# Kernel optimization log

Hardware: AMD Instinct MI355X
Metric: run time of the kernel (lower is better)

## Reference

```python
import jax, jax.numpy as jnp
import numpy as np

B, S, D = 16, 2048, 128

def setup_inputs() -> dict:
    key = jax.random.key(0)
    kq, kk, kv, km = jax.random.split(key, 4)
    Q = jax.random.normal(kq, (B, S, D), dtype=jnp.float32)
    K = jax.random.normal(kk, (B, S, D), dtype=jnp.float32)
    V = jax.random.normal(kv, (B, S, D), dtype=jnp.float32)
    # mask: True entries are masked out (filled with -inf), same as torch.masked_fill_
    mask = jax.random.randint(km, (B, S, S), 0, 2).astype(bool)
    return {"Q": Q, "K": K, "V": V, "mask": mask, "dk": 128}

def reference(Q, K, V, mask, dk):
    # scores: [B, S_q, S_k]
    w = jnp.einsum('bqd,bkd->bqk', Q, K)
    w = jnp.where(mask, -jnp.inf, w)
    # scale applied to masked scores (as in original: mask first, then divide);
    # -inf / scale stays -inf, so math matches exactly.
    scale = jnp.asarray(dk, w.dtype) ** 0.5
    p = jax.nn.softmax(w / scale, axis=-1)
    # context: [B, S_q, D]
    return jnp.einsum('bqk,bkd->bqd', p, V)
```

## Files before the change

kernel.cpp:

```cpp
#include <hip/hip_runtime.h>
#include <hip/hip_bf16.h>
#include <stdint.h>

typedef __attribute__((ext_vector_type(8))) short short8;
typedef __attribute__((ext_vector_type(4))) float floatx4;

#define S_LEN 2048
#define DH    128
#define BQ    64
#define BKV   64
#define NSTEP (S_LEN / BKV)
#define SCALE 0.08838834764831845f
#define SCALE2 0.12753785429791905f
#define DTHR 11.541560327111708f

__device__ __forceinline__ float ex2(float x) { return __builtin_amdgcn_exp2f(x); }

__device__ __forceinline__ unsigned short f2b(float f) {
    union { float f; unsigned u; } v; v.f = f;
    unsigned r = v.u + 0x7fffu + ((v.u >> 16) & 1u);
    return (unsigned short)(r >> 16);
}

__device__ __forceinline__ unsigned cvt_pk(float lo, float hi) {
    unsigned r;
    asm("v_cvt_pk_bf16_f32 %0, %1, %2" : "=v"(r) : "v"(lo), "v"(hi));
    return r;
}

__device__ __forceinline__ void gll16(const void* g, void* l) {
    __builtin_amdgcn_global_load_lds(
        (__attribute__((address_space(1))) void*)(g),
        (__attribute__((address_space(3))) void*)(l), 16, 0, 0);
}


__global__ __launch_bounds__(256) void conv_k(const float* __restrict__ K,
                                              unsigned short* __restrict__ Kbf)
{
    int i = blockIdx.x * 256 + threadIdx.x;
    float4 v = ((const float4*)K)[i];
    ushort4 o;
    o.x = f2b(v.x); o.y = f2b(v.y); o.z = f2b(v.z); o.w = f2b(v.w);
    ((ushort4*)Kbf)[i] = o;
}

__global__ __launch_bounds__(256) void transp_v(const float* __restrict__ V,
                                                unsigned short* __restrict__ Vt)
{
    __shared__ float t[32][33];
    const int k0 = blockIdx.x * 32, d0 = blockIdx.y * 32, b = blockIdx.z;
    const int tx = threadIdx.x & 31, ty = threadIdx.x >> 5;
    const float* Vb = V + ((size_t)b * S_LEN + k0) * DH + d0;
    #pragma unroll
    for (int i = 0; i < 4; ++i)
        t[ty + 8 * i][tx] = Vb[(size_t)(ty + 8 * i) * DH + tx];
    __syncthreads();
    unsigned short* Vtb = Vt + ((size_t)b * DH + d0) * S_LEN + k0;
    #pragma unroll
    for (int i = 0; i < 4; ++i)
        Vtb[(size_t)(ty + 8 * i) * S_LEN + tx] = f2b(t[tx][ty + 8 * i]);
}

#define LDS_BYTES 77824

__global__ __launch_bounds__(256, 2)
void attn_fwd(const float* __restrict__ Q, const unsigned short* __restrict__ Kbf,
              const unsigned short* __restrict__ Vt, const int* __restrict__ M,
              float* __restrict__ O)
{
    __shared__ __align__(128) char lds[LDS_BYTES];

    const int tid  = threadIdx.x;
    const int lane = tid & 63;
    const int w    = tid >> 6;
    const int c    = lane & 15;
    const int g    = lane >> 4;
    const int qt   = blockIdx.x;
    const int b    = blockIdx.y;
    const int q0   = qt * BQ;

    const int vd = tid & 127;
    const int vh = tid >> 7;
    const int krow_l = lane >> 4;
    const int kcol_l = (lane & 15) * 16;

    short8 qf[4];
    {
        const float* qrow = Q + ((size_t)(b * S_LEN + q0 + w * 16 + c)) * DH;
        #pragma unroll
        for (int dk = 0; dk < 4; ++dk) {
            const float* p = qrow + dk * 32 + g * 8;
            float4 a  = *(const float4*)(p);
            float4 bb = *(const float4*)(p + 4);
            short8 f;
            f[0] = f2b(a.x * SCALE2);  f[1] = f2b(a.y * SCALE2);
            f[2] = f2b(a.z * SCALE2);  f[3] = f2b(a.w * SCALE2);
            f[4] = f2b(bb.x * SCALE2); f[5] = f2b(bb.y * SCALE2);
            f[6] = f2b(bb.z * SCALE2); f[7] = f2b(bb.w * SCALE2);
            qf[dk] = f;
        }
    }

    float m_run = -1e30f;
    float l_run = 0.f;
    floatx4 accO[8];
    #pragma unroll
    for (int i = 0; i < 8; ++i) accO[i] = (floatx4)(0.f);

    const char*           Kb8 = (const char*)(Kbf + (size_t)b * S_LEN * DH);
    const unsigned short* Vtb = Vt + (size_t)b * DH * S_LEN;
    const int* Mrow = M + (size_t)b * S_LEN * S_LEN
                        + (size_t)(q0 + w * 16 + c) * S_LEN + 4 * g;

    short8 vreg[4];
    int4   mregA[4], mregB[4];
    char*  psw = lds + 69632 + w * 2048;

#define LOAD_MASK(DST, TT) {                                                  \
    const int* mp_ = Mrow + (TT) * BKV;                                       \
    DST[0] = *(const int4*)(mp_);                                             \
    DST[1] = *(const int4*)(mp_ + 16);                                        \
    DST[2] = *(const int4*)(mp_ + 32);                                        \
    DST[3] = *(const int4*)(mp_ + 48); }

    #pragma unroll
    for (int i = 0; i < 4; ++i) {
        int j = (w << 2) | i;
        int r = 4 * j + krow_l;
        unsigned cb = (unsigned)kcol_l ^ (unsigned)((r & 7) << 4);
        gll16(Kb8 + (size_t)r * 256 + cb, lds + j * 1024);
    }
    #pragma unroll
    for (int j = 0; j < 4; ++j)
        vreg[j] = *(const short8*)(Vtb + (size_t)vd * S_LEN + vh * 32 + j * 8);
    #pragma unroll
    for (int j = 0; j < 4; ++j)
        *(short8*)(lds + 32768 + vd * 144 + vh * 64 + j * 16) = vreg[j];
    #pragma unroll
    for (int j = 0; j < 4; ++j)
        vreg[j] = *(const short8*)(Vtb + (size_t)vd * S_LEN + BKV + vh * 32 + j * 8);
    LOAD_MASK(mregA, 0);
    LOAD_MASK(mregB, 1);
    __syncthreads();

#define STEP_BODY(T, MCUR) {                                                  \
    const int pb  = (T) & 1;                                                  \
    const int kv0 = (T) * BKV;                                                \
                 \
    if ((T) + 1 < NSTEP) {                                                    \
        const char* Ksrc = Kb8 + (size_t)(kv0 + BKV) * 256;                   \
        char* KHn = lds + ((pb ^ 1) * 16384);                                 \
        _Pragma("unroll")                                                     \
        for (int i = 0; i < 4; ++i) {                                         \
            int j = (w << 2) | i;                                             \
            int r = 4 * j + krow_l;                                           \
            unsigned cb = (unsigned)kcol_l ^ (unsigned)((r & 7) << 4);        \
            gll16(Ksrc + (size_t)r * 256 + cb, KHn + j * 1024);               \
        }                                                                     \
    }                                                                         \
                                       \
    if ((T) + 1 < NSTEP) {                                                    \
        _Pragma("unroll")                                                     \
        for (int j = 0; j < 4; ++j)                                           \
            *(short8*)(lds + 32768 + (pb ^ 1) * 18432 + vd * 144 + vh * 64    \
                       + j * 16) = vreg[j];                                   \
    }                                                                         \
                                                     \
    if ((T) + 2 < NSTEP) {                                                    \
        const unsigned short* vs_ = Vtb + (size_t)vd * S_LEN                  \
                                   + (kv0 + 2 * BKV) + vh * 32;               \
        _Pragma("unroll")                                                     \
        for (int j = 0; j < 4; ++j)                                           \
            vreg[j] = *(const short8*)(vs_ + j * 8);                          \
    }                                                                         \
                               \
    floatx4 accS[4];                                                          \
    _Pragma("unroll")                                                         \
    for (int n = 0; n < 4; ++n) accS[n] = (floatx4)(0.f);                     \
    {                                                                         \
        const char* KHp = lds + pb * 16384;                                   \
        __builtin_amdgcn_s_setprio(1);                                        \
        _Pragma("unroll")                                                     \
        for (int n = 0; n < 4; ++n) {                                         \
            const char* krow = KHp + (n * 16 + c) * 256;                      \
            _Pragma("unroll")                                                 \
            for (int dk = 0; dk < 4; ++dk) {                                  \
                short8 kf = *(const short8*)(krow +                           \
                    ((unsigned)(dk * 64 + g * 16) ^ (unsigned)((c & 7) << 4)));\
                accS[n] = __builtin_amdgcn_mfma_f32_16x16x32_bf16(            \
                              kf, qf[dk], accS[n], 0, 0, 0);                  \
            }                                                                 \
        }                                                                     \
        __builtin_amdgcn_s_setprio(0);                                        \
    }                                                                         \
                                \
    float p_[4][4];                                                           \
    _Pragma("unroll")                                                         \
    for (int n = 0; n < 4; ++n) {                                             \
        int4 mm = MCUR[n];                                                    \
        p_[n][0] = mm.x ? -1e30f : accS[n][0];                                \
        p_[n][1] = mm.y ? -1e30f : accS[n][1];                                \
        p_[n][2] = mm.z ? -1e30f : accS[n][2];                                \
        p_[n][3] = mm.w ? -1e30f : accS[n][3];                                \
    }                                                                         \
    float mx = p_[0][0];                                                      \
    _Pragma("unroll")                                                         \
    for (int n = 0; n < 4; ++n)                                               \
        _Pragma("unroll")                                                     \
        for (int r = 0; r < 4; ++r) mx = fmaxf(mx, p_[n][r]);                 \
    mx = fmaxf(mx, __shfl_xor(mx, 16));                                       \
    mx = fmaxf(mx, __shfl_xor(mx, 32));                                       \
    int need = __any(mx - m_run > DTHR);                                      \
    float corr = 1.0f;                                                        \
    if (need) {                                                               \
        float mn = fmaxf(m_run, mx);                                          \
        corr = ex2(m_run - mn);                                               \
        m_run = mn;                                                           \
    }                                                                         \
    float ts = 0.f;                                                           \
    _Pragma("unroll")                                                         \
    for (int n = 0; n < 4; ++n)                                               \
        _Pragma("unroll")                                                     \
        for (int r = 0; r < 4; ++r) {                                         \
            p_[n][r] = ex2(p_[n][r] - m_run);                                 \
            ts += p_[n][r];                                                   \
        }                                                                     \
    ts += __shfl_xor(ts, 16);                                                 \
    ts += __shfl_xor(ts, 32);                                                 \
    if (need) {                                                               \
        l_run = l_run * corr + ts;                                            \
        _Pragma("unroll")                                                     \
        for (int s8 = 0; s8 < 8; ++s8) {                                      \
            floatx4 o = accO[s8];                                             \
            o[0] *= corr; o[1] *= corr; o[2] *= corr; o[3] *= corr;           \
            accO[s8] = o;                                                     \
        }                                                                     \
    } else {                                                                  \
        l_run += ts;                                                          \
    }                                                                         \
                                                       \
    if ((T) + 2 < NSTEP) LOAD_MASK(MCUR, (T) + 2);                            \
                \
    _Pragma("unroll")                                                         \
    for (int n = 0; n < 4; ++n) {                                             \
        unsigned w0 = cvt_pk(p_[n][0], p_[n][1]);                             \
        unsigned w1 = cvt_pk(p_[n][2], p_[n][3]);                             \
        unsigned long long pk = (unsigned long long)w0                        \
                              | ((unsigned long long)w1 << 32);               \
        *(unsigned long long*)(psw + (4 * n + g) * 128                        \
                               + ((c * 8) ^ (g << 3))) = pk;                  \
    }                                                                         \
                     \
    {                                                                         \
        const char* VTp = lds + 32768 + pb * 18432;                           \
        _Pragma("unroll")                                                     \
        for (int sub = 0; sub < 2; ++sub) {                                   \
            int ra = 8 * sub + 2 * g;                                         \
            unsigned long long lo = *(const unsigned long long*)(psw + ra*128 \
                                    + ((c * 8) ^ ((ra & 3) << 3)));           \
            unsigned long long hi = *(const unsigned long long*)(psw          \
                                    + (ra + 1) * 128                          \
                                    + ((c * 8) ^ (((ra + 1) & 3) << 3)));     \
            union { unsigned long long q[2]; short8 v; } pu;                  \
            pu.q[0] = lo; pu.q[1] = hi;                                       \
            short8 pf = pu.v;                                                 \
            __builtin_amdgcn_s_setprio(1);                                    \
            _Pragma("unroll")                                                 \
            for (int s8 = 0; s8 < 8; ++s8) {                                  \
                short8 vf = *(const short8*)(VTp + (s8 * 16 + c) * 144        \
                                             + sub * 64 + g * 16);            \
                accO[s8] = __builtin_amdgcn_mfma_f32_16x16x32_bf16(           \
                               vf, pf, accO[s8], 0, 0, 0);                    \
            }                                                                 \
            __builtin_amdgcn_s_setprio(0);                                    \
        }                                                                     \
    }                                                                         \
    __syncthreads(); }

    for (int t = 0; t < NSTEP; t += 2) {
        STEP_BODY(t,     mregA)
        STEP_BODY(t + 1, mregB)
    }
#undef STEP_BODY
#undef LOAD_MASK

    float inv = (l_run > 0.f) ? 1.f / l_run : 0.f;
    float* Ob = O + ((size_t)(b * S_LEN + q0 + w * 16 + c)) * DH;
    #pragma unroll
    for (int s8 = 0; s8 < 8; ++s8) {
        float4 ov;
        ov.x = accO[s8][0] * inv; ov.y = accO[s8][1] * inv;
        ov.z = accO[s8][2] * inv; ov.w = accO[s8][3] * inv;
        *(float4*)(Ob + s8 * 16 + 4 * g) = ov;
    }
}

#define FB_LDS_BYTES 77824

__global__ __launch_bounds__(256, 2)
void attn_fwd_fb(const float* __restrict__ Q, const float* __restrict__ K,
                 const float* __restrict__ V, const int* __restrict__ M,
                 float* __restrict__ O)
{
    __shared__ __align__(128) char lds[FB_LDS_BYTES];

    const int tid  = threadIdx.x;
    const int lane = tid & 63;
    const int w    = tid >> 6;
    const int c    = lane & 15;
    const int g    = lane >> 4;
    const int qt   = blockIdx.x;
    const int b    = blockIdx.y;
    const int q0   = qt * BQ;

    const int rbase = tid >> 5;
    const int c4    = tid & 31;
    const unsigned swk = (unsigned)(c4 * 8) ^ (unsigned)(rbase << 4);
    const int vd    = tid & 127;
    const int vk0   = (tid >> 7) * 32;

    short8 qf[4];
    {
        const float* qrow = Q + ((size_t)(b * S_LEN + q0 + w * 16 + c)) * DH;
        #pragma unroll
        for (int dk = 0; dk < 4; ++dk) {
            const float* p = qrow + dk * 32 + g * 8;
            float4 a  = *(const float4*)(p);
            float4 bb = *(const float4*)(p + 4);
            short8 f;
            f[0] = f2b(a.x * SCALE);  f[1] = f2b(a.y * SCALE);
            f[2] = f2b(a.z * SCALE);  f[3] = f2b(a.w * SCALE);
            f[4] = f2b(bb.x * SCALE); f[5] = f2b(bb.y * SCALE);
            f[6] = f2b(bb.z * SCALE); f[7] = f2b(bb.w * SCALE);
            qf[dk] = f;
        }
    }

    float m_run[4] = {-1e30f, -1e30f, -1e30f, -1e30f};
    float l_run[4] = {0.f, 0.f, 0.f, 0.f};
    floatx4 accO[8];
    #pragma unroll
    for (int i = 0; i < 8; ++i) accO[i] = (floatx4)(0.f);

    const float* Kb = K + (size_t)b * S_LEN * DH;
    const float* Vb = V + (size_t)b * S_LEN * DH;
    const int*   Mb = M + (size_t)b * S_LEN * S_LEN + (size_t)q0 * S_LEN;

    size_t moff[4];
    #pragma unroll
    for (int r = 0; r < 4; ++r)
        moff[r] = (size_t)(w * 16 + 4 * g + r) * S_LEN;

    float4 kreg[8];
    float  vreg[32];
    int    mreg[16];

    #pragma unroll
    for (int i = 0; i < 8; ++i)
        kreg[i] = *(const float4*)(Kb + (size_t)(i * 8 + rbase) * DH + c4 * 4);
    #pragma unroll
    for (int j = 0; j < 32; ++j)
        vreg[j] = Vb[(size_t)(vk0 + j) * DH + vd];
    #pragma unroll
    for (int r = 0; r < 4; ++r)
        #pragma unroll
        for (int n = 0; n < 4; ++n)
            mreg[r * 4 + n] = Mb[moff[r] + n * 16 + c];

    #pragma unroll
    for (int i = 0; i < 8; ++i) {
        float4 kv = kreg[i];
        unsigned long long kp =
              (unsigned long long)f2b(kv.x)
            | ((unsigned long long)f2b(kv.y) << 16)
            | ((unsigned long long)f2b(kv.z) << 32)
            | ((unsigned long long)f2b(kv.w) << 48);
        *(unsigned long long*)(lds + (i * 8 + rbase) * 256 + swk) = kp;
    }
    {
        char* vbase = lds + 32768 + vd * 144 + vk0 * 2;
        #pragma unroll
        for (int i = 0; i < 4; ++i) {
            short8 pk;
            #pragma unroll
            for (int e = 0; e < 8; ++e) pk[e] = f2b(vreg[i * 8 + e]);
            *(short8*)(vbase + i * 16) = pk;
        }
    }
    #pragma unroll
    for (int i = 0; i < 8; ++i)
        kreg[i] = *(const float4*)(Kb + (size_t)(BKV + i * 8 + rbase) * DH + c4 * 4);
    #pragma unroll
    for (int j = 0; j < 32; ++j)
        vreg[j] = Vb[(size_t)(BKV + vk0 + j) * DH + vd];

    __syncthreads();

    char* psw = lds + 69632 + w * 2048;

    for (int step = 0; step < NSTEP; ++step) {
        const int p = step & 1;
        const int kv0 = step * BKV;
        char* KHp = lds + p * 16384;
        char* VTp = lds + 32768 + p * 18432;

        floatx4 accS[4];
        #pragma unroll
        for (int n = 0; n < 4; ++n) accS[n] = (floatx4)(0.f);
        #pragma unroll
        for (int n = 0; n < 4; ++n) {
            const char* krow = KHp + (n * 16 + c) * 256;
            #pragma unroll
            for (int dk = 0; dk < 4; ++dk) {
                unsigned colb = (unsigned)(dk * 64 + g * 16) ^ (unsigned)((c & 7) << 4);
                short8 kf = *(const short8*)(krow + colb);
                accS[n] = __builtin_amdgcn_mfma_f32_16x16x32_bf16(qf[dk], kf, accS[n], 0, 0, 0);
            }
        }

        float pv[4][4];
        float corr[4];
        #pragma unroll
        for (int r = 0; r < 4; ++r) {
            float sv[4];
            #pragma unroll
            for (int n = 0; n < 4; ++n) {
                float s = accS[n][r];
                if (mreg[r * 4 + n]) s = -1e30f;
                sv[n] = s;
            }
            float tm = fmaxf(fmaxf(sv[0], sv[1]), fmaxf(sv[2], sv[3]));
            #pragma unroll
            for (int off = 1; off < 16; off <<= 1)
                tm = fmaxf(tm, __shfl_xor(tm, off, 64));
            float mn = fmaxf(m_run[r], tm);
            corr[r]  = __expf(m_run[r] - mn);
            m_run[r] = mn;
            float ts = 0.f;
            #pragma unroll
            for (int n = 0; n < 4; ++n) { pv[n][r] = __expf(sv[n] - mn); ts += pv[n][r]; }
            #pragma unroll
            for (int off = 1; off < 16; off <<= 1)
                ts += __shfl_xor(ts, off, 64);
            l_run[r] = l_run[r] * corr[r] + ts;
        }
        if (step + 1 < NSTEP) {
            const int kvn = kv0 + BKV;
            #pragma unroll
            for (int r = 0; r < 4; ++r)
                #pragma unroll
                for (int n = 0; n < 4; ++n)
                    mreg[r * 4 + n] = Mb[moff[r] + kvn + n * 16 + c];
        }

        #pragma unroll
        for (int s8 = 0; s8 < 8; ++s8) {
            floatx4 o = accO[s8];
            o[0] *= corr[0]; o[1] *= corr[1]; o[2] *= corr[2]; o[3] *= corr[3];
            accO[s8] = o;
        }

        #pragma unroll
        for (int r = 0; r < 4; ++r) {
            int rl = 4 * g + r;
            #pragma unroll
            for (int n = 0; n < 4; ++n) {
                unsigned colb = (unsigned)((n * 16 + c) * 2) ^ (unsigned)((rl & 7) << 4);
                *(unsigned short*)(psw + rl * 128 + colb) = f2b(pv[n][r]);
            }
        }

        #pragma unroll
        for (int sub = 0; sub < 2; ++sub) {
            unsigned colb = (unsigned)(sub * 64 + g * 16) ^ (unsigned)((c & 7) << 4);
            short8 pf = *(const short8*)(psw + c * 128 + colb);
            #pragma unroll
            for (int s8 = 0; s8 < 8; ++s8) {
                short8 vf = *(const short8*)(VTp + (s8 * 16 + c) * 144 + sub * 64 + g * 16);
                accO[s8] = __builtin_amdgcn_mfma_f32_16x16x32_bf16(pf, vf, accO[s8], 0, 0, 0);
            }
        }

        if (step + 1 < NSTEP) {
            char* KHn = lds + (p ^ 1) * 16384;
            char* VTn = lds + 32768 + (p ^ 1) * 18432;
            #pragma unroll
            for (int i = 0; i < 8; ++i) {
                float4 kv = kreg[i];
                unsigned long long kp =
                      (unsigned long long)f2b(kv.x)
                    | ((unsigned long long)f2b(kv.y) << 16)
                    | ((unsigned long long)f2b(kv.z) << 32)
                    | ((unsigned long long)f2b(kv.w) << 48);
                *(unsigned long long*)(KHn + (i * 8 + rbase) * 256 + swk) = kp;
            }
            char* vbase = VTn + vd * 144 + vk0 * 2;
            #pragma unroll
            for (int i = 0; i < 4; ++i) {
                short8 pk;
                #pragma unroll
                for (int e = 0; e < 8; ++e) pk[e] = f2b(vreg[i * 8 + e]);
                *(short8*)(vbase + i * 16) = pk;
            }
            if (step + 2 < NSTEP) {
                const int kvn2 = kv0 + 2 * BKV;
                #pragma unroll
                for (int i = 0; i < 8; ++i)
                    kreg[i] = *(const float4*)(Kb + (size_t)(kvn2 + i * 8 + rbase) * DH + c4 * 4);
                #pragma unroll
                for (int j = 0; j < 32; ++j)
                    vreg[j] = Vb[(size_t)(kvn2 + vk0 + j) * DH + vd];
            }
        }
        __syncthreads();
    }

    float inv[4];
    #pragma unroll
    for (int r = 0; r < 4; ++r) inv[r] = (l_run[r] > 0.f) ? 1.f / l_run[r] : 0.f;
    float* Ob = O + ((size_t)(b * S_LEN + q0 + w * 16)) * DH;
    #pragma unroll
    for (int s8 = 0; s8 < 8; ++s8) {
        #pragma unroll
        for (int r = 0; r < 4; ++r) {
            Ob[(size_t)(4 * g + r) * DH + s8 * 16 + c] = accO[s8][r] * inv[r];
        }
    }
}

extern "C" void kernel_launch(void* const* d_in, const int* in_sizes, int n_in,
                              void* d_out, int out_size, void* d_ws, size_t ws_size,
                              hipStream_t stream) {
    const float* Q = (const float*)d_in[0];
    const float* K = (const float*)d_in[1];
    const float* V = (const float*)d_in[2];
    const int*   M = (const int*)d_in[3];
    float*       O = (float*)d_out;

    const size_t elems = (size_t)16 * S_LEN * DH;
    if (ws_size >= 2 * elems * sizeof(unsigned short)) {
        unsigned short* Kbf = (unsigned short*)d_ws;
        unsigned short* Vt  = (unsigned short*)d_ws + elems;
        conv_k<<<dim3((unsigned)(elems / 4 / 256)), dim3(256), 0, stream>>>(K, Kbf);
        transp_v<<<dim3(S_LEN / 32, DH / 32, 16), dim3(256), 0, stream>>>(V, Vt);
        attn_fwd<<<dim3(S_LEN / BQ, 16), dim3(256), 0, stream>>>(Q, Kbf, Vt, M, O);
    } else {
        attn_fwd_fb<<<dim3(S_LEN / BQ, 16), dim3(256), 0, stream>>>(Q, K, V, M, O);
    }
}
```

Baseline: 115.5 us.

## Double query rows per wave to reuse K/V tiles across two Q subtiles

Each wave now handles 32 query rows (two 16-row subtiles) instead of 16, so the block covers 128 queries and every K fragment and V fragment loaded from LDS feeds two MFMAs. This halves K/V global and LDS traffic per query. Mask prefetch changes from two-step-ahead double registers to one-step-ahead for both subtiles. In exchange, register pressure roughly doubles for accumulators, occupancy drops to one block per CU, and the grid halves to 256 blocks, which may underfill the GPU.

```diff
diff --git a/kernel.cpp b/kernel.cpp
--- a/kernel.cpp
+++ b/kernel.cpp
@@ -7,7 +7,7 @@
 
 #define S_LEN 2048
 #define DH    128
-#define BQ    64
+#define BQ    128
 #define BKV   64
 #define NSTEP (S_LEN / BKV)
 #define SCALE 0.08838834764831845f
@@ -62,9 +62,9 @@
         Vtb[(size_t)(ty + 8 * i) * S_LEN + tx] = f2b(t[tx][ty + 8 * i]);
 }
 
-#define LDS_BYTES 77824
-
-__global__ __launch_bounds__(256, 2)
+#define LDS_BYTES 86016
+
+__global__ __launch_bounds__(256, 1)
 void attn_fwd(const float* __restrict__ Q, const unsigned short* __restrict__ Kbf,
               const unsigned short* __restrict__ Vt, const int* __restrict__ M,
               float* __restrict__ O)
@@ -85,9 +85,10 @@
     const int krow_l = lane >> 4;
     const int kcol_l = (lane & 15) * 16;
 
-    short8 qf[4];
-    {
-        const float* qrow = Q + ((size_t)(b * S_LEN + q0 + w * 16 + c)) * DH;
+    short8 qf[2][4];
+    #pragma unroll
+    for (int qs = 0; qs < 2; ++qs) {
+        const float* qrow = Q + ((size_t)(b * S_LEN + q0 + w * 32 + qs * 16 + c)) * DH;
         #pragma unroll
         for (int dk = 0; dk < 4; ++dk) {
             const float* p = qrow + dk * 32 + g * 8;
@@ -98,31 +99,33 @@
             f[2] = f2b(a.z * SCALE2);  f[3] = f2b(a.w * SCALE2);
             f[4] = f2b(bb.x * SCALE2); f[5] = f2b(bb.y * SCALE2);
             f[6] = f2b(bb.z * SCALE2); f[7] = f2b(bb.w * SCALE2);
-            qf[dk] = f;
-        }
-    }
-
-    float m_run = -1e30f;
-    float l_run = 0.f;
-    floatx4 accO[8];
-    #pragma unroll
-    for (int i = 0; i < 8; ++i) accO[i] = (floatx4)(0.f);
+            qf[qs][dk] = f;
+        }
+    }
+
+    float m_run[2] = {-1e30f, -1e30f};
+    float l_run[2] = {0.f, 0.f};
+    floatx4 accO0[8], accO1[8];
+    #pragma unroll
+    for (int i = 0; i < 8; ++i) { accO0[i] = (floatx4)(0.f); accO1[i] = (floatx4)(0.f); }
 
     const char*           Kb8 = (const char*)(Kbf + (size_t)b * S_LEN * DH);
     const unsigned short* Vtb = Vt + (size_t)b * DH * S_LEN;
-    const int* Mrow = M + (size_t)b * S_LEN * S_LEN
-                        + (size_t)(q0 + w * 16 + c) * S_LEN + 4 * g;
+    const int* Mrow0 = M + (size_t)b * S_LEN * S_LEN
+                         + (size_t)(q0 + w * 32 + c) * S_LEN + 4 * g;
+    const int* Mrow1 = Mrow0 + (size_t)16 * S_LEN;
 
     short8 vreg[4];
-    int4   mregA[4], mregB[4];
-    char*  psw = lds + 69632 + w * 2048;
-
-#define LOAD_MASK(DST, TT) {                                                  \
-    const int* mp_ = Mrow + (TT) * BKV;                                       \
-    DST[0] = *(const int4*)(mp_);                                             \
-    DST[1] = *(const int4*)(mp_ + 16);                                        \
-    DST[2] = *(const int4*)(mp_ + 32);                                        \
-    DST[3] = *(const int4*)(mp_ + 48); }
+    int4   mcur[8];
+    char*  psw = lds + 69632 + w * 4096;
+
+#define LOAD_MASK(TT) {                                                       \
+    const int* m0_ = Mrow0 + (TT) * BKV;                                      \
+    const int* m1_ = Mrow1 + (TT) * BKV;                                      \
+    mcur[0] = *(const int4*)(m0_);      mcur[1] = *(const int4*)(m0_ + 16);   \
+    mcur[2] = *(const int4*)(m0_ + 32); mcur[3] = *(const int4*)(m0_ + 48);   \
+    mcur[4] = *(const int4*)(m1_);      mcur[5] = *(const int4*)(m1_ + 16);   \
+    mcur[6] = *(const int4*)(m1_ + 32); mcur[7] = *(const int4*)(m1_ + 48); }
 
     #pragma unroll
     for (int i = 0; i < 4; ++i) {
@@ -140,14 +143,13 @@
     #pragma unroll
     for (int j = 0; j < 4; ++j)
         vreg[j] = *(const short8*)(Vtb + (size_t)vd * S_LEN + BKV + vh * 32 + j * 8);
-    LOAD_MASK(mregA, 0);
-    LOAD_MASK(mregB, 1);
+    LOAD_MASK(0);
     __syncthreads();
 
-#define STEP_BODY(T, MCUR) {                                                  \
+#define STEP_BODY(T) {                                                        \
     const int pb  = (T) & 1;                                                  \
     const int kv0 = (T) * BKV;                                                \
-                 \
+                                                  \
     if ((T) + 1 < NSTEP) {                                                    \
         const char* Ksrc = Kb8 + (size_t)(kv0 + BKV) * 256;                   \
         char* KHn = lds + ((pb ^ 1) * 16384);                                 \
@@ -159,14 +161,13 @@
             gll16(Ksrc + (size_t)r * 256 + cb, KHn + j * 1024);               \
         }                                                                     \
     }                                                                         \
-                                       \
+                            \
     if ((T) + 1 < NSTEP) {                                                    \
         _Pragma("unroll")                                                     \
         for (int j = 0; j < 4; ++j)                                           \
             *(short8*)(lds + 32768 + (pb ^ 1) * 18432 + vd * 144 + vh * 64    \
                        + j * 16) = vreg[j];                                   \
     }                                                                         \
-                                                     \
     if ((T) + 2 < NSTEP) {                                                    \
         const unsigned short* vs_ = Vtb + (size_t)vd * S_LEN                  \
                                    + (kv0 + 2 * BKV) + vh * 32;               \
@@ -174,10 +175,11 @@
         for (int j = 0; j < 4; ++j)                                           \
             vreg[j] = *(const short8*)(vs_ + j * 8);                          \
     }                                                                         \
-                               \
-    floatx4 accS[4];                                                          \
+                                      \
+    floatx4 accS[2][4];                                                       \
     _Pragma("unroll")                                                         \
-    for (int n = 0; n < 4; ++n) accS[n] = (floatx4)(0.f);                     \
+    for (int n = 0; n < 4; ++n) { accS[0][n] = (floatx4)(0.f);                \
+                                  accS[1][n] = (floatx4)(0.f); }              \
     {                                                                         \
         const char* KHp = lds + pb * 16384;                                   \
         __builtin_amdgcn_s_setprio(1);                                        \
@@ -188,111 +190,134 @@
             for (int dk = 0; dk < 4; ++dk) {                                  \
                 short8 kf = *(const short8*)(krow +                           \
                     ((unsigned)(dk * 64 + g * 16) ^ (unsigned)((c & 7) << 4)));\
-                accS[n] = __builtin_amdgcn_mfma_f32_16x16x32_bf16(            \
-                              kf, qf[dk], accS[n], 0, 0, 0);                  \
+                accS[0][n] = __builtin_amdgcn_mfma_f32_16x16x32_bf16(         \
+                                 kf, qf[0][dk], accS[0][n], 0, 0, 0);         \
+                accS[1][n] = __builtin_amdgcn_mfma_f32_16x16x32_bf16(         \
+                                 kf, qf[1][dk], accS[1][n], 0, 0, 0);         \
             }                                                                 \
         }                                                                     \
         __builtin_amdgcn_s_setprio(0);                                        \
     }                                                                         \
-                                \
-    float p_[4][4];                                                           \
+                  \
     _Pragma("unroll")                                                         \
-    for (int n = 0; n < 4; ++n) {                                             \
-        int4 mm = MCUR[n];                                                    \
-        p_[n][0] = mm.x ? -1e30f : accS[n][0];                                \
-        p_[n][1] = mm.y ? -1e30f : accS[n][1];                                \
-        p_[n][2] = mm.z ? -1e30f : accS[n][2];                                \
-        p_[n][3] = mm.w ? -1e30f : accS[n][3];                                \
-    }                                                                         \
-    float mx = p_[0][0];                                                      \
-    _Pragma("unroll")                                                         \
-    for (int n = 0; n < 4; ++n)                                               \
-        _Pragma("unroll")                                                     \
-        for (int r = 0; r < 4; ++r) mx = fmaxf(mx, p_[n][r]);                 \
-    mx = fmaxf(mx, __shfl_xor(mx, 16));                                       \
-    mx = fmaxf(mx, __shfl_xor(mx, 32));                                       \
-    int need = __any(mx - m_run > DTHR);                                      \
-    float corr = 1.0f;                                                        \
-    if (need) {                                                               \
-        float mn = fmaxf(m_run, mx);                                          \
-        corr = ex2(m_run - mn);                                               \
-        m_run = mn;                                                           \
-    }                                                                         \
-    float ts = 0.f;                                                           \
-    _Pragma("unroll")                                                         \
-    for (int n = 0; n < 4; ++n)                                               \
-        _Pragma("unroll")                                                     \
-        for (int r = 0; r < 4; ++r) {                                         \
-            p_[n][r] = ex2(p_[n][r] - m_run);                                 \
-            ts += p_[n][r];                                                   \
-        }                                                                     \
-    ts += __shfl_xor(ts, 16);                                                 \
-    ts += __shfl_xor(ts, 32);                                                 \
-    if (need) {                                                               \
-        l_run = l_run * corr + ts;                                            \
-        _Pragma("unroll")                                                     \
-        for (int s8 = 0; s8 < 8; ++s8) {                                      \
-            floatx4 o = accO[s8];                                             \
-            o[0] *= corr; o[1] *= corr; o[2] *= corr; o[3] *= corr;           \
-            accO[s8] = o;                                                     \
-        }                                                                     \
-    } else {                                                                  \
-        l_run += ts;                                                          \
-    }                                                                         \
-                                                       \
-    if ((T) + 2 < NSTEP) LOAD_MASK(MCUR, (T) + 2);                            \
-                \
-    _Pragma("unroll")                                                         \
-    for (int n = 0; n < 4; ++n) {                                             \
-        unsigned w0 = cvt_pk(p_[n][0], p_[n][1]);                             \
-        unsigned w1 = cvt_pk(p_[n][2], p_[n][3]);                             \
-        unsigned long long pk = (unsigned long long)w0                        \
-                              | ((unsigned long long)w1 << 32);               \
-        *(unsigned long long*)(psw + (4 * n + g) * 128                        \
-                               + ((c * 8) ^ (g << 3))) = pk;                  \
+    for (int qs = 0; qs < 2; ++qs) {                                          \
+        float p_[4][4];                                                       \
+        _Pragma("unroll")                                                     \
+        for (int n = 0; n < 4; ++n) {                                         \
+            int4 mm = mcur[qs * 4 + n];                                       \
+            p_[n][0] = mm.x ? -1e30f : accS[qs][n][0];                        \
+            p_[n][1] = mm.y ? -1e30f : accS[qs][n][1];                        \
+            p_[n][2] = mm.z ? -1e30f : accS[qs][n][2];                        \
+            p_[n][3] = mm.w ? -1e30f : accS[qs][n][3];                        \
+        }                                                                     \
+        float mx = p_[0][0];                                                  \
+        _Pragma("unroll")                                                     \
+        for (int n = 0; n < 4; ++n)                                           \
+            _Pragma("unroll")                                                 \
+            for (int r = 0; r < 4; ++r) mx = fmaxf(mx, p_[n][r]);             \
+        mx = fmaxf(mx, __shfl_xor(mx, 16));                                   \
+        mx = fmaxf(mx, __shfl_xor(mx, 32));                                   \
+        int need = __any(mx - m_run[qs] > DTHR);                              \
+        float corr = 1.0f;                                                    \
+        if (need) {                                                           \
+            float mn = fmaxf(m_run[qs], mx);                                  \
+            corr = ex2(m_run[qs] - mn);                                       \
+            m_run[qs] = mn;                                                   \
+        }                                                                     \
+        float ts = 0.f;                                                       \
+        _Pragma("unroll")                                                     \
+        for (int n = 0; n < 4; ++n)                                           \
+            _Pragma("unroll")                                                 \
+            for (int r = 0; r < 4; ++r) {                                     \
+                p_[n][r] = ex2(p_[n][r] - m_run[qs]);                         \
+                ts += p_[n][r];                                               \
+            }                                                                 \
+        ts += __shfl_xor(ts, 16);                                             \
+        ts += __shfl_xor(ts, 32);                                             \
+        if (need) {                                                           \
+            l_run[qs] = l_run[qs] * corr + ts;                                \
+            if (qs == 0) {                                                    \
+                _Pragma("unroll")                                             \
+                for (int s8 = 0; s8 < 8; ++s8) {                              \
+                    floatx4 o = accO0[s8];                                    \
+                    o[0] *= corr; o[1] *= corr; o[2] *= corr; o[3] *= corr;   \
+                    accO0[s8] = o;                                            \
+                }                                                             \
+            } else {                                                          \
+                _Pragma("unroll")                                             \
+                for (int s8 = 0; s8 < 8; ++s8) {                              \
+                    floatx4 o = accO1[s8];                                    \
+                    o[0] *= corr; o[1] *= corr; o[2] *= corr; o[3] *= corr;   \
+                    accO1[s8] = o;                                            \
+                }                                                             \
+            }                                                                 \
+        } else {                                                              \
+            l_run[qs] += ts;                                                  \
+        }                                                                     \
+                  \
+        _Pragma("unroll")                                                     \
+        for (int n = 0; n < 4; ++n) {                                         \
+            unsigned w0 = cvt_pk(p_[n][0], p_[n][1]);                         \
+            unsigned w1 = cvt_pk(p_[n][2], p_[n][3]);                         \
+            unsigned long long pk = (unsigned long long)w0                    \
+                                  | ((unsigned long long)w1 << 32);           \
+            *(unsigned long long*)(psw + qs * 2048 + (4 * n + g) * 128        \
+                                   + ((c * 8) ^ (g << 3))) = pk;              \
+        }                                                                     \
     }                                                                         \
                      \
+    if ((T) + 1 < NSTEP) LOAD_MASK((T) + 1);                                  \
+                                        \
     {                                                                         \
         const char* VTp = lds + 32768 + pb * 18432;                           \
         _Pragma("unroll")                                                     \
         for (int sub = 0; sub < 2; ++sub) {                                   \
             int ra = 8 * sub + 2 * g;                                         \
-            unsigned long long lo = *(const unsigned long long*)(psw + ra*128 \
-                                    + ((c * 8) ^ ((ra & 3) << 3)));           \
-            unsigned long long hi = *(const unsigned long long*)(psw          \
-                                    + (ra + 1) * 128                          \
-                                    + ((c * 8) ^ (((ra + 1) & 3) << 3)));     \
-            union { unsigned long long q[2]; short8 v; } pu;                  \
-            pu.q[0] = lo; pu.q[1] = hi;                                       \
-            short8 pf = pu.v;                                                 \
+            short8 pf[2];                                                     \
+            _Pragma("unroll")                                                 \
+            for (int qs = 0; qs < 2; ++qs) {                                  \
+                unsigned long long lo = *(const unsigned long long*)(psw      \
+                    + qs * 2048 + ra * 128 + ((c * 8) ^ ((ra & 3) << 3)));    \
+                unsigned long long hi = *(const unsigned long long*)(psw      \
+                    + qs * 2048 + (ra + 1) * 128                              \
+                    + ((c * 8) ^ (((ra + 1) & 3) << 3)));                     \
+                union { unsigned long long q[2]; short8 v; } pu;              \
+                pu.q[0] = lo; pu.q[1] = hi;                                   \
+                pf[qs] = pu.v;                                                \
+            }                                                                 \
             __builtin_amdgcn_s_setprio(1);                                    \
             _Pragma("unroll")                                                 \
             for (int s8 = 0; s8 < 8; ++s8) {                                  \
                 short8 vf = *(const short8*)(VTp + (s8 * 16 + c) * 144        \
                                              + sub * 64 + g * 16);            \
-                accO[s8] = __builtin_amdgcn_mfma_f32_16x16x32_bf16(           \
-                               vf, pf, accO[s8], 0, 0, 0);                    \
+                accO0[s8] = __builtin_amdgcn_mfma_f32_16x16x32_bf16(          \
+                               vf, pf[0], accO0[s8], 0, 0, 0);                \
+                accO1[s8] = __builtin_amdgcn_mfma_f32_16x16x32_bf16(          \
+                               vf, pf[1], accO1[s8], 0, 0, 0);                \
             }                                                                 \
             __builtin_amdgcn_s_setprio(0);                                    \
         }                                                                     \
     }                                                                         \
     __syncthreads(); }
 
-    for (int t = 0; t < NSTEP; t += 2) {
-        STEP_BODY(t,     mregA)
-        STEP_BODY(t + 1, mregB)
+    for (int t = 0; t < NSTEP; ++t) {
+        STEP_BODY(t)
     }
 #undef STEP_BODY
 #undef LOAD_MASK
 
-    float inv = (l_run > 0.f) ? 1.f / l_run : 0.f;
-    float* Ob = O + ((size_t)(b * S_LEN + q0 + w * 16 + c)) * DH;
-    #pragma unroll
-    for (int s8 = 0; s8 < 8; ++s8) {
-        float4 ov;
-        ov.x = accO[s8][0] * inv; ov.y = accO[s8][1] * inv;
-        ov.z = accO[s8][2] * inv; ov.w = accO[s8][3] * inv;
-        *(float4*)(Ob + s8 * 16 + 4 * g) = ov;
+    #pragma unroll
+    for (int qs = 0; qs < 2; ++qs) {
+        float inv = (l_run[qs] > 0.f) ? 1.f / l_run[qs] : 0.f;
+        float* Ob = O + ((size_t)(b * S_LEN + q0 + w * 32 + qs * 16 + c)) * DH;
+        #pragma unroll
+        for (int s8 = 0; s8 < 8; ++s8) {
+            floatx4 a = qs ? accO1[s8] : accO0[s8];
+            float4 ov;
+            ov.x = a[0] * inv; ov.y = a[1] * inv;
+            ov.z = a[2] * inv; ov.w = a[3] * inv;
+            *(float4*)(Ob + s8 * 16 + 4 * g) = ov;
+        }
     }
 }
 
@@ -312,7 +337,7 @@
     const int g    = lane >> 4;
     const int qt   = blockIdx.x;
     const int b    = blockIdx.y;
-    const int q0   = qt * BQ;
+    const int q0   = qt * 64;
 
     const int rbase = tid >> 5;
     const int c4    = tid & 31;
@@ -546,6 +571,6 @@
         transp_v<<<dim3(S_LEN / 32, DH / 32, 16), dim3(256), 0, stream>>>(V, Vt);
         attn_fwd<<<dim3(S_LEN / BQ, 16), dim3(256), 0, stream>>>(Q, Kbf, Vt, M, O);
     } else {
-        attn_fwd_fb<<<dim3(S_LEN / BQ, 16), dim3(256), 0, stream>>>(Q, K, V, M, O);
-    }
-}
+        attn_fwd_fb<<<dim3(S_LEN / 64, 16), dim3(256), 0, stream>>>(Q, K, V, M, O);
+    }
+}
```

Result: slower. 126.9 us (+9.9%).

## Switch attention to 32x32 MFMA with KV-split waves and register P transpose

Applied to the files above, without the earlier changes.

Rewrites the main attention kernel to use 32x32x16 bf16 MFMA. The four waves are split into two query halves times two KV halves, and the two KV-half partial results are merged through LDS at the end. The P tile is repacked with cross-lane shuffles instead of a per-wave LDS round trip, which lets the P staging buffer be dropped and reduces LDS use. The intent is fewer MFMA and LDS instructions per step, at the cost of a final merge, larger accumulator register pressure, and mask loads now issued only one step ahead.

```diff
diff --git a/kernel.cpp b/kernel.cpp
--- a/kernel.cpp
+++ b/kernel.cpp
@@ -2,8 +2,9 @@
 #include <hip/hip_bf16.h>
 #include <stdint.h>
 
-typedef __attribute__((ext_vector_type(8))) short short8;
-typedef __attribute__((ext_vector_type(4))) float floatx4;
+typedef __attribute__((ext_vector_type(8)))  short short8;
+typedef __attribute__((ext_vector_type(4)))  float floatx4;
+typedef __attribute__((ext_vector_type(16))) float floatx16;
 
 #define S_LEN 2048
 #define DH    128
@@ -62,7 +63,7 @@
         Vtb[(size_t)(ty + 8 * i) * S_LEN + tx] = f2b(t[tx][ty + 8 * i]);
 }
 
-#define LDS_BYTES 77824
+#define LDS_BYTES 69632
 
 __global__ __launch_bounds__(256, 2)
 void attn_fwd(const float* __restrict__ Q, const unsigned short* __restrict__ Kbf,
@@ -70,6 +71,255 @@
               float* __restrict__ O)
 {
     __shared__ __align__(128) char lds[LDS_BYTES];
+
+    const int tid  = threadIdx.x;
+    const int lane = tid & 63;
+    const int w    = tid >> 6;
+    const int wq   = w & 1;
+    const int wk   = w >> 1;
+    const int lq   = lane & 31;
+    const int hi   = lane >> 5;
+    const int qt   = blockIdx.x;
+    const int b    = blockIdx.y;
+    const int q0   = qt * BQ;
+
+    const int vd = tid & 127;
+    const int vh = tid >> 7;
+    const int krow_l = lane >> 4;
+    const int kcol_l = (lane & 15) * 16;
+
+    short8 qf[8];
+    {
+        const float* qrow = Q + ((size_t)(b * S_LEN + q0 + wq * 32 + lq)) * DH;
+        #pragma unroll
+        for (int dsub = 0; dsub < 8; ++dsub) {
+            const float* p = qrow + dsub * 16 + hi * 8;
+            float4 a  = *(const float4*)(p);
+            float4 bb = *(const float4*)(p + 4);
+            short8 f;
+            f[0] = f2b(a.x * SCALE2);  f[1] = f2b(a.y * SCALE2);
+            f[2] = f2b(a.z * SCALE2);  f[3] = f2b(a.w * SCALE2);
+            f[4] = f2b(bb.x * SCALE2); f[5] = f2b(bb.y * SCALE2);
+            f[6] = f2b(bb.z * SCALE2); f[7] = f2b(bb.w * SCALE2);
+            qf[dsub] = f;
+        }
+    }
+
+    float m_run = -1e30f;
+    float l_run = 0.f;
+    floatx16 accO[4];
+    #pragma unroll
+    for (int i = 0; i < 4; ++i) accO[i] = (floatx16)(0.f);
+
+    const char*           Kb8 = (const char*)(Kbf + (size_t)b * S_LEN * DH);
+    const unsigned short* Vtb = Vt + (size_t)b * DH * S_LEN;
+    const int* Mrow = M + (size_t)b * S_LEN * S_LEN
+                        + (size_t)(q0 + wq * 32 + lq) * S_LEN + wk * 32 + 4 * hi;
+
+    short8 vreg[4];
+    int4   mcur[4];
+
+#define LOAD_MASK(TT) {                                                       \
+    const int* mp_ = Mrow + (TT) * BKV;                                       \
+    mcur[0] = *(const int4*)(mp_);                                            \
+    mcur[1] = *(const int4*)(mp_ + 8);                                        \
+    mcur[2] = *(const int4*)(mp_ + 16);                                       \
+    mcur[3] = *(const int4*)(mp_ + 24); }
+
+    #pragma unroll
+    for (int i = 0; i < 4; ++i) {
+        int j = (w << 2) | i;
+        int r = 4 * j + krow_l;
+        unsigned cb = (unsigned)kcol_l ^ (unsigned)((r & 15) << 4);
+        gll16(Kb8 + (size_t)r * 256 + cb, lds + j * 1024);
+    }
+    #pragma unroll
+    for (int j = 0; j < 4; ++j)
+        vreg[j] = *(const short8*)(Vtb + (size_t)vd * S_LEN + vh * 32 + j * 8);
+    #pragma unroll
+    for (int j = 0; j < 4; ++j)
+        *(short8*)(lds + 32768 + vd * 144 + vh * 64 + j * 16) = vreg[j];
+    #pragma unroll
+    for (int j = 0; j < 4; ++j)
+        vreg[j] = *(const short8*)(Vtb + (size_t)vd * S_LEN + BKV + vh * 32 + j * 8);
+    LOAD_MASK(0);
+    __syncthreads();
+
+#define STEP_BODY(T) {                                                        \
+    const int pb  = (T) & 1;                                                  \
+    const int kv0 = (T) * BKV;                                                \
+                                                  \
+    if ((T) + 1 < NSTEP) {                                                    \
+        const char* Ksrc = Kb8 + (size_t)(kv0 + BKV) * 256;                   \
+        char* KHn = lds + ((pb ^ 1) * 16384);                                 \
+        _Pragma("unroll")                                                     \
+        for (int i = 0; i < 4; ++i) {                                         \
+            int j = (w << 2) | i;                                             \
+            int r = 4 * j + krow_l;                                           \
+            unsigned cb = (unsigned)kcol_l ^ (unsigned)((r & 15) << 4);       \
+            gll16(Ksrc + (size_t)r * 256 + cb, KHn + j * 1024);               \
+        }                                                                     \
+    }                                                                         \
+                            \
+    if ((T) + 1 < NSTEP) {                                                    \
+        _Pragma("unroll")                                                     \
+        for (int j = 0; j < 4; ++j)                                           \
+            *(short8*)(lds + 32768 + (pb ^ 1) * 18432 + vd * 144 + vh * 64    \
+                       + j * 16) = vreg[j];                                   \
+    }                                                                         \
+    if ((T) + 2 < NSTEP) {                                                    \
+        const unsigned short* vs_ = Vtb + (size_t)vd * S_LEN                  \
+                                   + (kv0 + 2 * BKV) + vh * 32;               \
+        _Pragma("unroll")                                                     \
+        for (int j = 0; j < 4; ++j)                                           \
+            vreg[j] = *(const short8*)(vs_ + j * 8);                          \
+    }                                                                         \
+            \
+    floatx16 accS = (floatx16)(0.f);                                          \
+    {                                                                         \
+        const char* KHp = lds + pb * 16384;                                   \
+        const int krow = wk * 32 + lq;                                        \
+        const char* kbase = KHp + krow * 256;                                 \
+        const unsigned ksw = (unsigned)((krow & 15) << 4);                    \
+        __builtin_amdgcn_s_setprio(1);                                        \
+        _Pragma("unroll")                                                     \
+        for (int dsub = 0; dsub < 8; ++dsub) {                                \
+            short8 kf = *(const short8*)(kbase +                              \
+                ((unsigned)(dsub * 32 + hi * 16) ^ ksw));                     \
+            accS = __builtin_amdgcn_mfma_f32_32x32x16_bf16(                   \
+                       kf, qf[dsub], accS, 0, 0, 0);                          \
+        }                                                                     \
+        __builtin_amdgcn_s_setprio(0);                                        \
+    }                                                                         \
+      \
+    float p_[16];                                                             \
+    _Pragma("unroll")                                                         \
+    for (int j = 0; j < 4; ++j) {                                             \
+        int4 mm = mcur[j];                                                    \
+        p_[4*j+0] = mm.x ? -1e30f : accS[4*j+0];                              \
+        p_[4*j+1] = mm.y ? -1e30f : accS[4*j+1];                              \
+        p_[4*j+2] = mm.z ? -1e30f : accS[4*j+2];                              \
+        p_[4*j+3] = mm.w ? -1e30f : accS[4*j+3];                              \
+    }                                                                         \
+    float mx = p_[0];                                                         \
+    _Pragma("unroll")                                                         \
+    for (int r = 1; r < 16; ++r) mx = fmaxf(mx, p_[r]);                       \
+    mx = fmaxf(mx, __shfl_xor(mx, 32));                                       \
+    int need = __any(mx - m_run > DTHR);                                      \
+    float corr = 1.0f;                                                        \
+    if (need) {                                                               \
+        float mn = fmaxf(m_run, mx);                                          \
+        corr = ex2(m_run - mn);                                               \
+        m_run = mn;                                                           \
+    }                                                                         \
+    float ts = 0.f;                                                           \
+    _Pragma("unroll")                                                         \
+    for (int r = 0; r < 16; ++r) { p_[r] = ex2(p_[r] - m_run); ts += p_[r]; } \
+    ts += __shfl_xor(ts, 32);                                                 \
+    if (need) {                                                               \
+        l_run = l_run * corr + ts;                                            \
+        _Pragma("unroll")                                                     \
+        for (int ds = 0; ds < 4; ++ds) {                                      \
+            floatx16 o = accO[ds];                                            \
+            _Pragma("unroll")                                                 \
+            for (int r = 0; r < 16; ++r) o[r] *= corr;                        \
+            accO[ds] = o;                                                     \
+        }                                                                     \
+    } else {                                                                  \
+        l_run += ts;                                                          \
+    }                                                                         \
+    if ((T) + 1 < NSTEP) LOAD_MASK((T) + 1);                                  \
+              \
+    short8 pf[2];                                                             \
+    _Pragma("unroll")                                                         \
+    for (int ks = 0; ks < 2; ++ks) {                                          \
+        unsigned a01 = cvt_pk(p_[8*ks+0], p_[8*ks+1]);                        \
+        unsigned a23 = cvt_pk(p_[8*ks+2], p_[8*ks+3]);                        \
+        unsigned b01 = cvt_pk(p_[8*ks+4], p_[8*ks+5]);                        \
+        unsigned b23 = cvt_pk(p_[8*ks+6], p_[8*ks+7]);                        \
+        unsigned ta01 = (unsigned)__shfl_xor((int)a01, 32);                   \
+        unsigned ta23 = (unsigned)__shfl_xor((int)a23, 32);                   \
+        unsigned tb01 = (unsigned)__shfl_xor((int)b01, 32);                   \
+        unsigned tb23 = (unsigned)__shfl_xor((int)b23, 32);                   \
+        union { unsigned u[4]; short8 v; } pu;                                \
+        pu.u[0] = hi ? tb01 : a01;                                            \
+        pu.u[1] = hi ? tb23 : a23;                                            \
+        pu.u[2] = hi ? b01 : ta01;                                            \
+        pu.u[3] = hi ? b23 : ta23;                                            \
+        pf[ks] = pu.v;                                                        \
+    }                                                                         \
+           \
+    {                                                                         \
+        const char* VTp = lds + 32768 + pb * 18432;                           \
+        __builtin_amdgcn_s_setprio(1);                                        \
+        _Pragma("unroll")                                                     \
+        for (int ds = 0; ds < 4; ++ds) {                                      \
+            const char* vbase = VTp + (ds * 32 + lq) * 144 + wk * 64 + hi*16; \
+            _Pragma("unroll")                                                 \
+            for (int ks = 0; ks < 2; ++ks) {                                  \
+                short8 vf = *(const short8*)(vbase + ks * 32);                \
+                accO[ds] = __builtin_amdgcn_mfma_f32_32x32x16_bf16(           \
+                               vf, pf[ks], accO[ds], 0, 0, 0);                \
+            }                                                                 \
+        }                                                                     \
+        __builtin_amdgcn_s_setprio(0);                                        \
+    }                                                                         \
+    __syncthreads(); }
+
+    for (int t = 0; t < NSTEP; ++t) {
+        STEP_BODY(t)
+    }
+#undef STEP_BODY
+#undef LOAD_MASK
+
+    {
+        float* mg = (float*)lds;
+        const int slot = (wq * 64 + lane) * 68;
+        if (wk == 1) {
+            #pragma unroll
+            for (int ds = 0; ds < 4; ++ds)
+                #pragma unroll
+                for (int rr = 0; rr < 4; ++rr) {
+                    float4 v;
+                    v.x = accO[ds][4*rr+0]; v.y = accO[ds][4*rr+1];
+                    v.z = accO[ds][4*rr+2]; v.w = accO[ds][4*rr+3];
+                    *(float4*)(mg + slot + ds * 16 + rr * 4) = v;
+                }
+            mg[slot + 64] = m_run;
+            mg[slot + 65] = l_run;
+        }
+        __syncthreads();
+        if (wk == 0) {
+            float m1 = mg[slot + 64], l1 = mg[slot + 65];
+            float m  = fmaxf(m_run, m1);
+            float f0 = ex2(m_run - m), f1 = ex2(m1 - m);
+            float l  = l_run * f0 + l1 * f1;
+            float inv = (l > 0.f) ? 1.f / l : 0.f;
+            float* Ob = O + ((size_t)(b * S_LEN + q0 + wq * 32 + lq)) * DH;
+            #pragma unroll
+            for (int ds = 0; ds < 4; ++ds)
+                #pragma unroll
+                for (int rr = 0; rr < 4; ++rr) {
+                    float4 part = *(const float4*)(mg + slot + ds * 16 + rr * 4);
+                    float4 ov;
+                    ov.x = (accO[ds][4*rr+0] * f0 + part.x * f1) * inv;
+                    ov.y = (accO[ds][4*rr+1] * f0 + part.y * f1) * inv;
+                    ov.z = (accO[ds][4*rr+2] * f0 + part.z * f1) * inv;
+                    ov.w = (accO[ds][4*rr+3] * f0 + part.w * f1) * inv;
+                    *(float4*)(Ob + ds * 32 + 8 * rr + 4 * hi) = ov;
+                }
+        }
+    }
+}
+
+#define FB_LDS_BYTES 77824
+
+__global__ __launch_bounds__(256, 2)
+void attn_fwd_fb(const float* __restrict__ Q, const float* __restrict__ K,
+                 const float* __restrict__ V, const int* __restrict__ M,
+                 float* __restrict__ O)
+{
+    __shared__ __align__(128) char lds[FB_LDS_BYTES];
 
     const int tid  = threadIdx.x;
     const int lane = tid & 63;
@@ -78,241 +328,7 @@
     const int g    = lane >> 4;
     const int qt   = blockIdx.x;
     const int b    = blockIdx.y;
-    const int q0   = qt * BQ;
-
-    const int vd = tid & 127;
-    const int vh = tid >> 7;
-    const int krow_l = lane >> 4;
-    const int kcol_l = (lane & 15) * 16;
-
-    short8 qf[4];
-    {
-        const float* qrow = Q + ((size_t)(b * S_LEN + q0 + w * 16 + c)) * DH;
-        #pragma unroll
-        for (int dk = 0; dk < 4; ++dk) {
-            const float* p = qrow + dk * 32 + g * 8;
-            float4 a  = *(const float4*)(p);
-            float4 bb = *(const float4*)(p + 4);
-            short8 f;
-            f[0] = f2b(a.x * SCALE2);  f[1] = f2b(a.y * SCALE2);
-            f[2] = f2b(a.z * SCALE2);  f[3] = f2b(a.w * SCALE2);
-            f[4] = f2b(bb.x * SCALE2); f[5] = f2b(bb.y * SCALE2);
-            f[6] = f2b(bb.z * SCALE2); f[7] = f2b(bb.w * SCALE2);
-            qf[dk] = f;
-        }
-    }
-
-    float m_run = -1e30f;
-    float l_run = 0.f;
-    floatx4 accO[8];
-    #pragma unroll
-    for (int i = 0; i < 8; ++i) accO[i] = (floatx4)(0.f);
-
-    const char*           Kb8 = (const char*)(Kbf + (size_t)b * S_LEN * DH);
-    const unsigned short* Vtb = Vt + (size_t)b * DH * S_LEN;
-    const int* Mrow = M + (size_t)b * S_LEN * S_LEN
-                        + (size_t)(q0 + w * 16 + c) * S_LEN + 4 * g;
-
-    short8 vreg[4];
-    int4   mregA[4], mregB[4];
-    char*  psw = lds + 69632 + w * 2048;
-
-#define LOAD_MASK(DST, TT) {                                                  \
-    const int* mp_ = Mrow + (TT) * BKV;                                       \
-    DST[0] = *(const int4*)(mp_);                                             \
-    DST[1] = *(const int4*)(mp_ + 16);                                        \
-    DST[2] = *(const int4*)(mp_ + 32);                                        \
-    DST[3] = *(const int4*)(mp_ + 48); }
-
-    #pragma unroll
-    for (int i = 0; i < 4; ++i) {
-        int j = (w << 2) | i;
-        int r = 4 * j + krow_l;
-        unsigned cb = (unsigned)kcol_l ^ (unsigned)((r & 7) << 4);
-        gll16(Kb8 + (size_t)r * 256 + cb, lds + j * 1024);
-    }
-    #pragma unroll
-    for (int j = 0; j < 4; ++j)
-        vreg[j] = *(const short8*)(Vtb + (size_t)vd * S_LEN + vh * 32 + j * 8);
-    #pragma unroll
-    for (int j = 0; j < 4; ++j)
-        *(short8*)(lds + 32768 + vd * 144 + vh * 64 + j * 16) = vreg[j];
-    #pragma unroll
-    for (int j = 0; j < 4; ++j)
-        vreg[j] = *(const short8*)(Vtb + (size_t)vd * S_LEN + BKV + vh * 32 + j * 8);
-    LOAD_MASK(mregA, 0);
-    LOAD_MASK(mregB, 1);
-    __syncthreads();
-
-#define STEP_BODY(T, MCUR) {                                                  \
-    const int pb  = (T) & 1;                                                  \
-    const int kv0 = (T) * BKV;                                                \
-                 \
-    if ((T) + 1 < NSTEP) {                                                    \
-        const char* Ksrc = Kb8 + (size_t)(kv0 + BKV) * 256;                   \
-        char* KHn = lds + ((pb ^ 1) * 16384);                                 \
-        _Pragma("unroll")                                                     \
-        for (int i = 0; i < 4; ++i) {                                         \
-            int j = (w << 2) | i;                                             \
-            int r = 4 * j + krow_l;                                           \
-            unsigned cb = (unsigned)kcol_l ^ (unsigned)((r & 7) << 4);        \
-            gll16(Ksrc + (size_t)r * 256 + cb, KHn + j * 1024);               \
-        }                                                                     \
-    }                                                                         \
-                                       \
-    if ((T) + 1 < NSTEP) {                                                    \
-        _Pragma("unroll")                                                     \
-        for (int j = 0; j < 4; ++j)                                           \
-            *(short8*)(lds + 32768 + (pb ^ 1) * 18432 + vd * 144 + vh * 64    \
-                       + j * 16) = vreg[j];                                   \
-    }                                                                         \
-                                                     \
-    if ((T) + 2 < NSTEP) {                                                    \
-        const unsigned short* vs_ = Vtb + (size_t)vd * S_LEN                  \
-                                   + (kv0 + 2 * BKV) + vh * 32;               \
-        _Pragma("unroll")                                                     \
-        for (int j = 0; j < 4; ++j)                                           \
-            vreg[j] = *(const short8*)(vs_ + j * 8);                          \
-    }                                                                         \
-                               \
-    floatx4 accS[4];                                                          \
-    _Pragma("unroll")                                                         \
-    for (int n = 0; n < 4; ++n) accS[n] = (floatx4)(0.f);                     \
-    {                                                                         \
-        const char* KHp = lds + pb * 16384;                                   \
-        __builtin_amdgcn_s_setprio(1);                                        \
-        _Pragma("unroll")                                                     \
-        for (int n = 0; n < 4; ++n) {                                         \
-            const char* krow = KHp + (n * 16 + c) * 256;                      \
-            _Pragma("unroll")                                                 \
-            for (int dk = 0; dk < 4; ++dk) {                                  \
-                short8 kf = *(const short8*)(krow +                           \
-                    ((unsigned)(dk * 64 + g * 16) ^ (unsigned)((c & 7) << 4)));\
-                accS[n] = __builtin_amdgcn_mfma_f32_16x16x32_bf16(            \
-                              kf, qf[dk], accS[n], 0, 0, 0);                  \
-            }                                                                 \
-        }                                                                     \
-        __builtin_amdgcn_s_setprio(0);                                        \
-    }                                                                         \
-                                \
-    float p_[4][4];                                                           \
-    _Pragma("unroll")                                                         \
-    for (int n = 0; n < 4; ++n) {                                             \
-        int4 mm = MCUR[n];                                                    \
-        p_[n][0] = mm.x ? -1e30f : accS[n][0];                                \
-        p_[n][1] = mm.y ? -1e30f : accS[n][1];                                \
-        p_[n][2] = mm.z ? -1e30f : accS[n][2];                                \
-        p_[n][3] = mm.w ? -1e30f : accS[n][3];                                \
-    }                                                                         \
-    float mx = p_[0][0];                                                      \
-    _Pragma("unroll")                                                         \
-    for (int n = 0; n < 4; ++n)                                               \
-        _Pragma("unroll")                                                     \
-        for (int r = 0; r < 4; ++r) mx = fmaxf(mx, p_[n][r]);                 \
-    mx = fmaxf(mx, __shfl_xor(mx, 16));                                       \
-    mx = fmaxf(mx, __shfl_xor(mx, 32));                                       \
-    int need = __any(mx - m_run > DTHR);                                      \
-    float corr = 1.0f;                                                        \
-    if (need) {                                                               \
-        float mn = fmaxf(m_run, mx);                                          \
-        corr = ex2(m_run - mn);                                               \
-        m_run = mn;                                                           \
-    }                                                                         \
-    float ts = 0.f;                                                           \
-    _Pragma("unroll")                                                         \
-    for (int n = 0; n < 4; ++n)                                               \
-        _Pragma("unroll")                                                     \
-        for (int r = 0; r < 4; ++r) {                                         \
-            p_[n][r] = ex2(p_[n][r] - m_run);                                 \
-            ts += p_[n][r];                                                   \
-        }                                                                     \
-    ts += __shfl_xor(ts, 16);                                                 \
-    ts += __shfl_xor(ts, 32);                                                 \
-    if (need) {                                                               \
-        l_run = l_run * corr + ts;                                            \
-        _Pragma("unroll")                                                     \
-        for (int s8 = 0; s8 < 8; ++s8) {                                      \
-            floatx4 o = accO[s8];                                             \
-            o[0] *= corr; o[1] *= corr; o[2] *= corr; o[3] *= corr;           \
-            accO[s8] = o;                                                     \
-        }                                                                     \
-    } else {                                                                  \
-        l_run += ts;                                                          \
-    }                                                                         \
-                                                       \
-    if ((T) + 2 < NSTEP) LOAD_MASK(MCUR, (T) + 2);                            \
-                \
-    _Pragma("unroll")                                                         \
-    for (int n = 0; n < 4; ++n) {                                             \
-        unsigned w0 = cvt_pk(p_[n][0], p_[n][1]);                             \
-        unsigned w1 = cvt_pk(p_[n][2], p_[n][3]);                             \
-        unsigned long long pk = (unsigned long long)w0                        \
-                              | ((unsigned long long)w1 << 32);               \
-        *(unsigned long long*)(psw + (4 * n + g) * 128                        \
-                               + ((c * 8) ^ (g << 3))) = pk;                  \
-    }                                                                         \
-                     \
-    {                                                                         \
-        const char* VTp = lds + 32768 + pb * 18432;                           \
-        _Pragma("unroll")                                                     \
-        for (int sub = 0; sub < 2; ++sub) {                                   \
-            int ra = 8 * sub + 2 * g;                                         \
-            unsigned long long lo = *(const unsigned long long*)(psw + ra*128 \
-                                    + ((c * 8) ^ ((ra & 3) << 3)));           \
-            unsigned long long hi = *(const unsigned long long*)(psw          \
-                                    + (ra + 1) * 128                          \
-                                    + ((c * 8) ^ (((ra + 1) & 3) << 3)));     \
-            union { unsigned long long q[2]; short8 v; } pu;                  \
-            pu.q[0] = lo; pu.q[1] = hi;                                       \
-            short8 pf = pu.v;                                                 \
-            __builtin_amdgcn_s_setprio(1);                                    \
-            _Pragma("unroll")                                                 \
-            for (int s8 = 0; s8 < 8; ++s8) {                                  \
-                short8 vf = *(const short8*)(VTp + (s8 * 16 + c) * 144        \
-                                             + sub * 64 + g * 16);            \
-                accO[s8] = __builtin_amdgcn_mfma_f32_16x16x32_bf16(           \
-                               vf, pf, accO[s8], 0, 0, 0);                    \
-            }                                                                 \
-            __builtin_amdgcn_s_setprio(0);                                    \
-        }                                                                     \
-    }                                                                         \
-    __syncthreads(); }
-
-    for (int t = 0; t < NSTEP; t += 2) {
-        STEP_BODY(t,     mregA)
-        STEP_BODY(t + 1, mregB)
-    }
-#undef STEP_BODY
-#undef LOAD_MASK
-
-    float inv = (l_run > 0.f) ? 1.f / l_run : 0.f;
-    float* Ob = O + ((size_t)(b * S_LEN + q0 + w * 16 + c)) * DH;
-    #pragma unroll
-    for (int s8 = 0; s8 < 8; ++s8) {
-        float4 ov;
-        ov.x = accO[s8][0] * inv; ov.y = accO[s8][1] * inv;
-        ov.z = accO[s8][2] * inv; ov.w = accO[s8][3] * inv;
-        *(float4*)(Ob + s8 * 16 + 4 * g) = ov;
-    }
-}
-
-#define FB_LDS_BYTES 77824
-
-__global__ __launch_bounds__(256, 2)
-void attn_fwd_fb(const float* __restrict__ Q, const float* __restrict__ K,
-                 const float* __restrict__ V, const int* __restrict__ M,
-                 float* __restrict__ O)
-{
-    __shared__ __align__(128) char lds[FB_LDS_BYTES];
-
-    const int tid  = threadIdx.x;
-    const int lane = tid & 63;
-    const int w    = tid >> 6;
-    const int c    = lane & 15;
-    const int g    = lane >> 4;
-    const int qt   = blockIdx.x;
-    const int b    = blockIdx.y;
-    const int q0   = qt * BQ;
+    const int q0   = qt * 64;
 
     const int rbase = tid >> 5;
     const int c4    = tid & 31;
@@ -546,6 +562,6 @@
         transp_v<<<dim3(S_LEN / 32, DH / 32, 16), dim3(256), 0, stream>>>(V, Vt);
         attn_fwd<<<dim3(S_LEN / BQ, 16), dim3(256), 0, stream>>>(Q, Kbf, Vt, M, O);
     } else {
-        attn_fwd_fb<<<dim3(S_LEN / BQ, 16), dim3(256), 0, stream>>>(Q, K, V, M, O);
-    }
-}
+        attn_fwd_fb<<<dim3(S_LEN / 64, 16), dim3(256), 0, stream>>>(Q, K, V, M, O);
+    }
+}
```

New measurement: 118.5 us. 1.03x slower.
